# Kernel optimization log

Hardware: AMD Instinct MI355X
Metric: run time of the kernel (lower is better)

Reference implementation:

```python
import jax, jax.numpy as jnp
import numpy as np

D_MODEL = 1024
N_HEADS = 16
D_K = D_MODEL // N_HEADS
B, S = 2, 2048
NEG = -1000000000.0


def setup_inputs() -> dict:
    key = jax.random.key(0)
    ks = jax.random.split(key, 11)
    scale = 1.0 / np.sqrt(D_MODEL)
    inp = {
        'q': jax.random.normal(ks[0], (B, S, D_MODEL), jnp.float32),
        'k': jax.random.normal(ks[1], (B, S, D_MODEL), jnp.float32),
        'v': jax.random.normal(ks[2], (B, S, D_MODEL), jnp.float32),
        'mask': jnp.tril(jnp.ones((S, S), dtype=bool))[None, None],  # causal [1,1,S,S]
        'w_q': jax.random.normal(ks[3], (D_MODEL, D_MODEL), jnp.float32) * scale,
        'b_q': jax.random.normal(ks[4], (D_MODEL,), jnp.float32) * 0.01,
        'w_k': jax.random.normal(ks[5], (D_MODEL, D_MODEL), jnp.float32) * scale,
        'b_k': jax.random.normal(ks[6], (D_MODEL,), jnp.float32) * 0.01,
        'w_v': jax.random.normal(ks[7], (D_MODEL, D_MODEL), jnp.float32) * scale,
        'b_v': jax.random.normal(ks[8], (D_MODEL,), jnp.float32) * 0.01,
        'w_o': jax.random.normal(ks[9], (D_MODEL, D_MODEL), jnp.float32) * scale,
        'b_o': jax.random.normal(ks[10], (D_MODEL,), jnp.float32) * 0.01,
    }
    return inp


def _split_heads(x):
    b, s, _ = x.shape
    return x.reshape(b, s, N_HEADS, D_K).transpose(0, 2, 1, 3)  # [b,h,s,dk]


def reference(q, k, v, mask, w_q, b_q, w_k, b_k, w_v, b_v, w_o, b_o):
    # Linear projections (torch Linear: x @ W.T + b)
    qh = _split_heads(q @ w_q.T + b_q)
    kh = _split_heads(k @ w_k.T + b_k)
    vh = _split_heads(v @ w_v.T + b_v)
    # scaled dot-product attention (dropout is identity in eval)
    scores = jnp.einsum('bhqd,bhkd->bhqk', qh, kh) / jnp.sqrt(jnp.float32(D_K))
    scores = jnp.where(mask, scores, NEG)
    attn_weights = jax.nn.softmax(scores, axis=-1)
    out = jnp.einsum('bhqk,bhkd->bhqd', attn_weights, vh)
    out = out.transpose(0, 2, 1, 3).reshape(q.shape[0], -1, D_MODEL)
    out = out @ w_o.T + b_o
    return out, attn_weights
```

## Files before the change

### kernel.cpp

```cpp
#include <hip/hip_runtime.h>
#include <hip/hip_bf16.h>


#define DM 1024
#define NH 16
#define DKH 64
#define BB 2
#define SS 2048
#define MM (BB*SS)

typedef __bf16 bf16_t;
typedef __bf16 bf16x4 __attribute__((ext_vector_type(4)));
typedef __bf16 bf16x8 __attribute__((ext_vector_type(8)));
typedef float  f32x4  __attribute__((ext_vector_type(4)));

#define EXP2F(x) __builtin_amdgcn_exp2f(x)

__device__ __forceinline__ f32x4 mfma16(bf16x8 a, bf16x8 b, f32x4 c) {
    return __builtin_amdgcn_mfma_f32_16x16x32_bf16(a, b, c, 0, 0, 0);
}
__device__ __forceinline__ bf16x8 cat8(bf16x4 lo, bf16x4 hi) {
    bf16x8 r;
    r[0]=lo[0]; r[1]=lo[1]; r[2]=lo[2]; r[3]=lo[3];
    r[4]=hi[0]; r[5]=hi[1]; r[6]=hi[2]; r[7]=hi[3];
    return r;
}

__device__ __forceinline__ void gload16(const bf16_t* g, bf16_t* l) {
    __builtin_amdgcn_global_load_lds(
        (const __attribute__((address_space(1))) void*)g,
        (__attribute__((address_space(3))) void*)l, 16, 0, 0);
}

__device__ __forceinline__ bf16x8 ldsw(const bf16_t* t, int row, int ch) {
    return *(const bf16x8*)(t + row * 64 + (((ch ^ row) & 7) << 3));
}

__global__ __launch_bounds__(256)
void cvt_bf16(const float* __restrict__ s0, const float* __restrict__ s1,
              const float* __restrict__ s2, const float* __restrict__ s3,
              bf16_t* __restrict__ d0, bf16_t* __restrict__ d1,
              bf16_t* __restrict__ d2, bf16_t* __restrict__ d3)
{
    const float* ss[4] = {s0, s1, s2, s3};
    bf16_t*      dd[4] = {d0, d1, d2, d3};
    const float* s = ss[blockIdx.y];
    bf16_t*      d = dd[blockIdx.y];
    size_t i = (size_t)(blockIdx.x * 256 + threadIdx.x) * 8;
    float4 f0 = *(const float4*)(s + i);
    float4 f1 = *(const float4*)(s + i + 4);
    bf16x8 v;
    v[0]=(bf16_t)f0.x; v[1]=(bf16_t)f0.y; v[2]=(bf16_t)f0.z; v[3]=(bf16_t)f0.w;
    v[4]=(bf16_t)f1.x; v[5]=(bf16_t)f1.y; v[6]=(bf16_t)f1.z; v[7]=(bf16_t)f1.w;
    *(bf16x8*)(d + i) = v;
}

template<int MODE>
__global__ __launch_bounds__(256)
void mha_gemm5(const bf16_t* __restrict__ A, const bf16_t* __restrict__ W,
               const float* __restrict__ bias, void* __restrict__ out)
{
    __shared__ bf16_t As[2][128 * 64];
    __shared__ bf16_t Bs[2][64 * 64];

    const int tid  = threadIdx.x;
    const int lane = tid & 63;
    const int wid  = tid >> 6;
    const int wm = wid >> 1, wn = wid & 1;
    const int bid  = blockIdx.x;
    const int xcd  = bid & 7, slot = bid >> 3;
    const int bm   = xcd * 4 + (slot >> 4);
    const int bn   = slot & 15;
    const int c = lane & 15, g = lane >> 4;
    const int sr = tid >> 3, sch = tid & 7;
    const int scol = ((sch ^ (sr & 7)) << 3);

    f32x4 acc[4][2] = {};

    const bf16_t* Ab = A + (size_t)(bm * 128 + sr) * DM + scol;
    const bf16_t* Wb = W + (size_t)(bn * 64 + sr) * DM + scol;

#define GSTAGE(buf, kt)  do {                                              \
        bf16_t* asl = &As[buf][wid * 512];                                 \
        bf16_t* bsl = &Bs[buf][wid * 512];                                 \
        _Pragma("unroll")                                                  \
        for (int j = 0; j < 4; ++j)                                        \
            gload16(Ab + (size_t)(j * 32) * DM + (kt) * 64, asl + j * 2048);\
        _Pragma("unroll")                                                  \
        for (int j = 0; j < 2; ++j)                                        \
            gload16(Wb + (size_t)(j * 32) * DM + (kt) * 64, bsl + j * 2048);\
    } while (0)

    GSTAGE(0, 0);
    for (int kt = 0; kt < DM / 64; ++kt) {
        const int cur = kt & 1;
        __syncthreads();
        if (kt + 1 < DM / 64) GSTAGE(cur ^ 1, kt + 1);
        const bf16_t* as = As[cur];
        const bf16_t* bs = Bs[cur];
        #pragma unroll
        for (int kh = 0; kh < 2; ++kh) {
            bf16x8 am[4], bw[2];
            #pragma unroll
            for (int f = 0; f < 4; ++f)
                am[f] = ldsw(as, wm * 64 + f * 16 + c, kh * 4 + g);
            #pragma unroll
            for (int f = 0; f < 2; ++f)
                bw[f] = ldsw(bs, wn * 32 + f * 16 + c, kh * 4 + g);
            #pragma unroll
            for (int fm = 0; fm < 4; ++fm)
                #pragma unroll
                for (int fn = 0; fn < 2; ++fn)
                    acc[fm][fn] = mfma16(am[fm], bw[fn], acc[fm][fn]);
        }
    }
#undef GSTAGE

    #pragma unroll
    for (int fm = 0; fm < 4; ++fm) {
        #pragma unroll
        for (int fn = 0; fn < 2; ++fn) {
            const int col = bn * 64 + wn * 32 + fn * 16 + c;
            const float bcol = bias[col];
            if constexpr (MODE == 2) {
                const int h = (col >> 6) & 15, dk = col & 63;
                const int row0 = bm * 128 + wm * 64 + fm * 16 + 4 * g;
                const int b = row0 >> 11, s0 = row0 & (SS - 1);
                bf16x4 pv;
                #pragma unroll
                for (int r = 0; r < 4; ++r) pv[r] = (bf16_t)(acc[fm][fn][r] + bcol);
                size_t idx = ((size_t)((b * NH + h) * DKH + dk)) * SS
                           + ((s0 >> 5) << 5) + g * 8 + (fm & 1) * 4;
                *(bf16x4*)&((bf16_t*)out)[idx] = pv;
            } else {
                #pragma unroll
                for (int r = 0; r < 4; ++r) {
                    const int row = bm * 128 + wm * 64 + fm * 16 + 4 * g + r;
                    float val = acc[fm][fn][r] + bcol;
                    if constexpr (MODE == 3) {
                        __builtin_nontemporal_store(
                            val, &((float*)out)[(size_t)row * DM + col]);
                    } else {
                        if constexpr (MODE == 0)
                            val *= 0.125f * 1.44269504f;
                        const int b = row >> 11, s = row & (SS - 1);
                        const int h = (col >> 6) & 15;
                        const int fnl = (col >> 4) & 3;
                        const int pos = ((fnl >> 1) << 5) + ((c >> 2) << 3)
                                      + ((fnl & 1) << 2) + (c & 3);
                        ((bf16_t*)out)[((size_t)(b * NH + h) * SS + s) * DKH + pos]
                            = (bf16_t)val;
                    }
                }
            }
        }
    }
}

__global__ __launch_bounds__(256)
void mha_attn11(const bf16_t* __restrict__ Qp, const bf16_t* __restrict__ Kp,
                const bf16_t* __restrict__ Vt, float* __restrict__ attn,
                bf16_t* __restrict__ aout)
{
    __shared__ bf16_t Ks[2][8192];
    __shared__ bf16_t Vs[2][8192];

    const int tid = threadIdx.x, lane = tid & 63, w = tid >> 6;
    const int c = lane & 15, g = lane >> 4;
    const int jb = blockIdx.x, bh = blockIdx.y;
    const int b = bh >> 4, h = bh & 15;

    const bf16_t* Qb = Qp + (size_t)bh * SS * DKH;
    const bf16_t* Kb = Kp + (size_t)bh * SS * DKH;
    const bf16_t* Vb = Vt + (size_t)bh * DKH * SS;
    float* attb = attn + (size_t)bh * SS * SS;

    const int sr = tid >> 3, sch = tid & 7;
    const int ssw = ((sch ^ (sr & 7)) << 3);

    #pragma unroll 1
    for (int half = 0; half < 2; ++half) {
        const int qt = half ? (31 - jb) : jb;
        const int q0 = qt * 64, q0w = q0 + w * 16;
        const int ntile = qt + 1;
        const int nr = (ntile + 1) >> 1;

        const bf16_t* qrow = Qb + (size_t)(q0w + c) * DKH;
        const bf16x8 qa0 = *(const bf16x8*)(qrow + g * 8);
        const bf16x8 qa1 = *(const bf16x8*)(qrow + 32 + g * 8);

#define STAGE_K(buf, rr) do {                                               \
        const bf16_t* s0_ = Kb + (size_t)(2 * (rr)) * 4096 + sr * 64 + ssw; \
        gload16(s0_,        &Ks[buf][w * 512]);                             \
        gload16(s0_ + 2048, &Ks[buf][2048 + w * 512]);                      \
        gload16(s0_ + 4096, &Ks[buf][4096 + w * 512]);                      \
        gload16(s0_ + 6144, &Ks[buf][6144 + w * 512]);                      \
    } while (0)

#define STAGE_V(buf, rr) do {                                               \
        const bf16_t* v0_ = Vb + (size_t)sr * SS + (2 * (rr)) * 64 + ssw;   \
        gload16(v0_,                        &Vs[buf][w * 512]);             \
        gload16(v0_ + (size_t)32 * SS,      &Vs[buf][2048 + w * 512]);      \
        gload16(v0_ + 64,                   &Vs[buf][4096 + w * 512]);      \
        gload16(v0_ + (size_t)32 * SS + 64, &Vs[buf][6144 + w * 512]);      \
    } while (0)

        __syncthreads();
        STAGE_K(0, 0);
        float lsum = 0.f;
        for (int rr = 0; rr < nr; ++rr) {
            const int cur = rr & 1;
            __syncthreads();
            if (rr + 1 < nr) STAGE_K(cur ^ 1, rr + 1);
            #pragma unroll
            for (int t = 0; t < 2; ++t) {
                const int kt = 2 * rr + t;
                if (kt < ntile) {
                    const bf16_t* ks = &Ks[cur][t * 4096];
                    f32x4 s[4] = {};
                    #pragma unroll
                    for (int sb = 0; sb < 4; ++sb) {
                        bf16x8 k0 = ldsw(ks, sb * 16 + c, g);
                        bf16x8 k1 = ldsw(ks, sb * 16 + c, 4 | g);
                        s[sb] = mfma16(k0, qa0, s[sb]);
                        s[sb] = mfma16(k1, qa1, s[sb]);
                    }
                    if (kt == qt) {
                        #pragma unroll
                        for (int sb = 0; sb < 4; ++sb)
                            #pragma unroll
                            for (int r = 0; r < 4; ++r)
                                if (sb * 16 + 4 * g + r <= w * 16 + c)
                                    lsum += EXP2F(s[sb][r]);
                    } else {
                        #pragma unroll
                        for (int sb = 0; sb < 4; ++sb)
                            #pragma unroll
                            for (int r = 0; r < 4; ++r)
                                lsum += EXP2F(s[sb][r]);
                    }
                }
            }
        }
        lsum += __shfl_xor(lsum, 16);
        lsum += __shfl_xor(lsum, 32);
        const float invl = 1.f / lsum;

        __syncthreads();
        STAGE_K(0, 0);
        STAGE_V(0, 0);
        f32x4 o[4] = {};
        for (int rr = 0; rr < nr; ++rr) {
            const int cur = rr & 1;
            __syncthreads();
            if (rr + 1 < nr) {
                STAGE_K(cur ^ 1, rr + 1);
                STAGE_V(cur ^ 1, rr + 1);
            }
            #pragma unroll
            for (int t = 0; t < 2; ++t) {
                const int kt = 2 * rr + t;
                if (kt < ntile) {
                    const bf16_t* ks = &Ks[cur][t * 4096];
                    const bf16_t* vs = &Vs[cur][t * 4096];
                    f32x4 s[4] = {};
                    #pragma unroll
                    for (int sb = 0; sb < 4; ++sb) {
                        bf16x8 k0 = ldsw(ks, sb * 16 + c, g);
                        bf16x8 k1 = ldsw(ks, sb * 16 + c, 4 | g);
                        s[sb] = mfma16(k0, qa0, s[sb]);
                        s[sb] = mfma16(k1, qa1, s[sb]);
                    }
                    const bool diag = (kt == qt);
                    bf16x4 pb[4];
                    float* prow = attb + (size_t)(q0w + c) * SS + kt * 64 + 4 * g;
                    #pragma unroll
                    for (int sb = 0; sb < 4; ++sb) {
                        f32x4 pf;
                        #pragma unroll
                        for (int r = 0; r < 4; ++r) {
                            bool msk = diag && (sb * 16 + 4 * g + r > w * 16 + c);
                            float p = msk ? 0.f : EXP2F(s[sb][r]) * invl;
                            pf[r] = p;
                            pb[sb][r] = (bf16_t)p;
                        }
                        *(f32x4*)(prow + sb * 16) = pf;
                    }
                    const bf16x8 pa0 = cat8(pb[0], pb[1]);
                    const bf16x8 pa1 = cat8(pb[2], pb[3]);
                    #pragma unroll
                    for (int fn = 0; fn < 4; ++fn) {
                        bf16x8 v0 = ldsw(vs, fn * 16 + c, g);
                        bf16x8 v1 = ldsw(vs, fn * 16 + c, 4 | g);
                        o[fn] = mfma16(pa0, v0, o[fn]);
                        o[fn] = mfma16(pa1, v1, o[fn]);
                    }
                }
            }
        }
#undef STAGE_K
#undef STAGE_V

        #pragma unroll
        for (int fn = 0; fn < 4; ++fn)
            #pragma unroll
            for (int r = 0; r < 4; ++r)
                aout[(size_t)(b * SS + q0w + 4 * g + r) * DM + h * DKH + fn * 16 + c]
                    = (bf16_t)o[fn][r];

        {
            const int zr = q0 + (tid >> 2);
            f32x4 z = {0.f, 0.f, 0.f, 0.f};
            float* dst = attb + (size_t)zr * SS;
            for (int col = ntile * 64 + (tid & 3) * 4; col < SS; col += 16)
                *(f32x4*)(dst + col) = z;
        }
    }
}

extern "C" void kernel_launch(void* const* d_in, const int* in_sizes, int n_in,
                              void* d_out, int out_size, void* d_ws, size_t ws_size,
                              hipStream_t stream)
{
    const float* q   = (const float*)d_in[0];
    const float* k   = (const float*)d_in[1];
    const float* v   = (const float*)d_in[2];
    const float* w_q = (const float*)d_in[4];
    const float* b_q = (const float*)d_in[5];
    const float* w_k = (const float*)d_in[6];
    const float* b_k = (const float*)d_in[7];
    const float* w_v = (const float*)d_in[8];
    const float* b_v = (const float*)d_in[9];
    const float* w_o = (const float*)d_in[10];
    const float* b_o = (const float*)d_in[11];

    float* out   = (float*)d_out;
    float* attnw = out + (size_t)MM * DM;

    bf16_t* Qp   = (bf16_t*)d_ws;
    bf16_t* Kp   = Qp + (size_t)MM * DM;
    bf16_t* Vt   = Kp + (size_t)MM * DM;
    bf16_t* aout = Vt + (size_t)MM * DM;
    bf16_t* qb   = aout + (size_t)MM * DM;
    bf16_t* kb   = qb + (size_t)MM * DM;
    bf16_t* vb   = kb + (size_t)MM * DM;
    bf16_t* wqb  = vb + (size_t)MM * DM;
    bf16_t* wkb  = wqb + (size_t)DM * DM;
    bf16_t* wvb  = wkb + (size_t)DM * DM;
    bf16_t* wob  = wvb + (size_t)DM * DM;

    cvt_bf16<<<dim3(MM * DM / 2048, 3), 256, 0, stream>>>(q, k, v, q, qb, kb, vb, qb);
    cvt_bf16<<<dim3(DM * DM / 2048, 4), 256, 0, stream>>>(w_q, w_k, w_v, w_o,
                                                          wqb, wkb, wvb, wob);

    mha_gemm5<0><<<512, 256, 0, stream>>>(qb, wqb, b_q, Qp);
    mha_gemm5<1><<<512, 256, 0, stream>>>(kb, wkb, b_k, Kp);
    mha_gemm5<2><<<512, 256, 0, stream>>>(vb, wvb, b_v, Vt);

    mha_attn11<<<dim3(16, BB * NH), 256, 0, stream>>>(Qp, Kp, Vt, attnw, aout);

    mha_gemm5<3><<<512, 256, 0, stream>>>(aout, wob, b_o, out);
}
```

Measured before the change: 256.2 us.

## Process paired query tiles jointly to share K/V staging in attention

The attention kernel used to handle its two query tiles (jb and 31-jb) one after the other, staging K and V from global memory separately for each. It now walks the K/V tiles once for the longer tile and computes both query tiles against each staged tile, so the shorter tile reuses the shared-memory data. This cuts global K/V loads and barrier rounds roughly in half. In exchange it holds two accumulator sets and two Q fragments per thread, which raises register pressure and may lower occupancy.

```diff
diff --git a/kernel.cpp b/kernel.cpp
--- a/kernel.cpp
+++ b/kernel.cpp
@@ -158,7 +158,7 @@
 }
 
 __global__ __launch_bounds__(256)
-void mha_attn11(const bf16_t* __restrict__ Qp, const bf16_t* __restrict__ Kp,
+void mha_attn12(const bf16_t* __restrict__ Qp, const bf16_t* __restrict__ Kp,
                 const bf16_t* __restrict__ Vt, float* __restrict__ attn,
                 bf16_t* __restrict__ aout)
 {
@@ -170,6 +170,12 @@
     const int jb = blockIdx.x, bh = blockIdx.y;
     const int b = bh >> 4, h = bh & 15;
 
+    const int qtA = jb, qtB = 31 - jb;
+    const int q0A = qtA * 64, q0B = qtB * 64;
+    const int q0wA = q0A + w * 16, q0wB = q0B + w * 16;
+    const int ntA = qtA + 1, ntB = qtB + 1;
+    const int nr = (ntB + 1) >> 1;
+
     const bf16_t* Qb = Qp + (size_t)bh * SS * DKH;
     const bf16_t* Kb = Kp + (size_t)bh * SS * DKH;
     const bf16_t* Vb = Vt + (size_t)bh * DKH * SS;
@@ -178,16 +184,12 @@
     const int sr = tid >> 3, sch = tid & 7;
     const int ssw = ((sch ^ (sr & 7)) << 3);
 
-    #pragma unroll 1
-    for (int half = 0; half < 2; ++half) {
-        const int qt = half ? (31 - jb) : jb;
-        const int q0 = qt * 64, q0w = q0 + w * 16;
-        const int ntile = qt + 1;
-        const int nr = (ntile + 1) >> 1;
-
-        const bf16_t* qrow = Qb + (size_t)(q0w + c) * DKH;
-        const bf16x8 qa0 = *(const bf16x8*)(qrow + g * 8);
-        const bf16x8 qa1 = *(const bf16x8*)(qrow + 32 + g * 8);
+    const bf16_t* qrA = Qb + (size_t)(q0wA + c) * DKH;
+    const bf16x8 qaA0 = *(const bf16x8*)(qrA + g * 8);
+    const bf16x8 qaA1 = *(const bf16x8*)(qrA + 32 + g * 8);
+    const bf16_t* qrB = Qb + (size_t)(q0wB + c) * DKH;
+    const bf16x8 qaB0 = *(const bf16x8*)(qrB + g * 8);
+    const bf16x8 qaB1 = *(const bf16x8*)(qrB + 32 + g * 8);
 
 #define STAGE_K(buf, rr) do {                                               \
         const bf16_t* s0_ = Kb + (size_t)(2 * (rr)) * 4096 + sr * 64 + ssw; \
@@ -205,82 +207,111 @@
         gload16(v0_ + (size_t)32 * SS + 64, &Vs[buf][6144 + w * 512]);      \
     } while (0)
 
+    STAGE_K(0, 0);
+    float lsumA = 0.f, lsumB = 0.f;
+    for (int rr = 0; rr < nr; ++rr) {
+        const int cur = rr & 1;
         __syncthreads();
-        STAGE_K(0, 0);
-        float lsum = 0.f;
-        for (int rr = 0; rr < nr; ++rr) {
-            const int cur = rr & 1;
-            __syncthreads();
-            if (rr + 1 < nr) STAGE_K(cur ^ 1, rr + 1);
-            #pragma unroll
-            for (int t = 0; t < 2; ++t) {
-                const int kt = 2 * rr + t;
-                if (kt < ntile) {
-                    const bf16_t* ks = &Ks[cur][t * 4096];
+        if (rr + 1 < nr) STAGE_K(cur ^ 1, rr + 1);
+        #pragma unroll
+        for (int t = 0; t < 2; ++t) {
+            const int kt = 2 * rr + t;
+            if (kt < ntB) {
+                const bf16_t* ks = &Ks[cur][t * 4096];
+                {
                     f32x4 s[4] = {};
                     #pragma unroll
                     for (int sb = 0; sb < 4; ++sb) {
                         bf16x8 k0 = ldsw(ks, sb * 16 + c, g);
                         bf16x8 k1 = ldsw(ks, sb * 16 + c, 4 | g);
-                        s[sb] = mfma16(k0, qa0, s[sb]);
-                        s[sb] = mfma16(k1, qa1, s[sb]);
-                    }
-                    if (kt == qt) {
+                        s[sb] = mfma16(k0, qaB0, s[sb]);
+                        s[sb] = mfma16(k1, qaB1, s[sb]);
+                    }
+                    if (kt == qtB) {
                         #pragma unroll
                         for (int sb = 0; sb < 4; ++sb)
                             #pragma unroll
                             for (int r = 0; r < 4; ++r)
                                 if (sb * 16 + 4 * g + r <= w * 16 + c)
-                                    lsum += EXP2F(s[sb][r]);
+                                    lsumB += EXP2F(s[sb][r]);
                     } else {
                         #pragma unroll
                         for (int sb = 0; sb < 4; ++sb)
                             #pragma unroll
                             for (int r = 0; r < 4; ++r)
-                                lsum += EXP2F(s[sb][r]);
+                                lsumB += EXP2F(s[sb][r]);
+                    }
+                }
+                if (kt < ntA) {
+                    f32x4 s[4] = {};
+                    #pragma unroll
+                    for (int sb = 0; sb < 4; ++sb) {
+                        bf16x8 k0 = ldsw(ks, sb * 16 + c, g);
+                        bf16x8 k1 = ldsw(ks, sb * 16 + c, 4 | g);
+                        s[sb] = mfma16(k0, qaA0, s[sb]);
+                        s[sb] = mfma16(k1, qaA1, s[sb]);
+                    }
+                    if (kt == qtA) {
+                        #pragma unroll
+                        for (int sb = 0; sb < 4; ++sb)
+                            #pragma unroll
+                            for (int r = 0; r < 4; ++r)
+                                if (sb * 16 + 4 * g + r <= w * 16 + c)
+                                    lsumA += EXP2F(s[sb][r]);
+                    } else {
+                        #pragma unroll
+                        for (int sb = 0; sb < 4; ++sb)
+                            #pragma unroll
+                            for (int r = 0; r < 4; ++r)
+                                lsumA += EXP2F(s[sb][r]);
                     }
                 }
             }
         }
-        lsum += __shfl_xor(lsum, 16);
-        lsum += __shfl_xor(lsum, 32);
-        const float invl = 1.f / lsum;
-
+    }
+    lsumA += __shfl_xor(lsumA, 16);
+    lsumA += __shfl_xor(lsumA, 32);
+    lsumB += __shfl_xor(lsumB, 16);
+    lsumB += __shfl_xor(lsumB, 32);
+    const float invlA = 1.f / lsumA;
+    const float invlB = 1.f / lsumB;
+
+    __syncthreads();
+    STAGE_K(0, 0);
+    STAGE_V(0, 0);
+    f32x4 oA[4] = {}, oB[4] = {};
+    for (int rr = 0; rr < nr; ++rr) {
+        const int cur = rr & 1;
         __syncthreads();
-        STAGE_K(0, 0);
-        STAGE_V(0, 0);
-        f32x4 o[4] = {};
-        for (int rr = 0; rr < nr; ++rr) {
-            const int cur = rr & 1;
-            __syncthreads();
-            if (rr + 1 < nr) {
-                STAGE_K(cur ^ 1, rr + 1);
-                STAGE_V(cur ^ 1, rr + 1);
-            }
-            #pragma unroll
-            for (int t = 0; t < 2; ++t) {
-                const int kt = 2 * rr + t;
-                if (kt < ntile) {
-                    const bf16_t* ks = &Ks[cur][t * 4096];
-                    const bf16_t* vs = &Vs[cur][t * 4096];
+        if (rr + 1 < nr) {
+            STAGE_K(cur ^ 1, rr + 1);
+            STAGE_V(cur ^ 1, rr + 1);
+        }
+        #pragma unroll
+        for (int t = 0; t < 2; ++t) {
+            const int kt = 2 * rr + t;
+            if (kt < ntB) {
+                const bf16_t* ks = &Ks[cur][t * 4096];
+                const bf16_t* vs = &Vs[cur][t * 4096];
+                {
                     f32x4 s[4] = {};
                     #pragma unroll
                     for (int sb = 0; sb < 4; ++sb) {
                         bf16x8 k0 = ldsw(ks, sb * 16 + c, g);
                         bf16x8 k1 = ldsw(ks, sb * 16 + c, 4 | g);
-                        s[sb] = mfma16(k0, qa0, s[sb]);
-                        s[sb] = mfma16(k1, qa1, s[sb]);
-                    }
-                    const bool diag = (kt == qt);
+                        s[sb] = mfma16(k0, qaB0, s[sb]);
+                        s[sb] = mfma16(k1, qaB1, s[sb]);
+                    }
+                    const bool diag = (kt == qtB);
                     bf16x4 pb[4];
-                    float* prow = attb + (size_t)(q0w + c) * SS + kt * 64 + 4 * g;
+                    float* prow = attb + (size_t)(q0wB + c) * SS + kt * 64 + 4 * g;
                     #pragma unroll
                     for (int sb = 0; sb < 4; ++sb) {
                         f32x4 pf;
                         #pragma unroll
                         for (int r = 0; r < 4; ++r) {
                             bool msk = diag && (sb * 16 + 4 * g + r > w * 16 + c);
-                            float p = msk ? 0.f : EXP2F(s[sb][r]) * invl;
+                            float p = msk ? 0.f : EXP2F(s[sb][r]) * invlB;
                             pf[r] = p;
                             pb[sb][r] = (bf16_t)p;
                         }
@@ -292,27 +323,72 @@
                     for (int fn = 0; fn < 4; ++fn) {
                         bf16x8 v0 = ldsw(vs, fn * 16 + c, g);
                         bf16x8 v1 = ldsw(vs, fn * 16 + c, 4 | g);
-                        o[fn] = mfma16(pa0, v0, o[fn]);
-                        o[fn] = mfma16(pa1, v1, o[fn]);
+                        oB[fn] = mfma16(pa0, v0, oB[fn]);
+                        oB[fn] = mfma16(pa1, v1, oB[fn]);
+                    }
+                }
+                if (kt < ntA) {
+                    f32x4 s[4] = {};
+                    #pragma unroll
+                    for (int sb = 0; sb < 4; ++sb) {
+                        bf16x8 k0 = ldsw(ks, sb * 16 + c, g);
+                        bf16x8 k1 = ldsw(ks, sb * 16 + c, 4 | g);
+                        s[sb] = mfma16(k0, qaA0, s[sb]);
+                        s[sb] = mfma16(k1, qaA1, s[sb]);
+                    }
+                    const bool diag = (kt == qtA);
+                    bf16x4 pb[4];
+                    float* prow = attb + (size_t)(q0wA + c) * SS + kt * 64 + 4 * g;
+                    #pragma unroll
+                    for (int sb = 0; sb < 4; ++sb) {
+                        f32x4 pf;
+                        #pragma unroll
+                        for (int r = 0; r < 4; ++r) {
+                            bool msk = diag && (sb * 16 + 4 * g + r > w * 16 + c);
+                            float p = msk ? 0.f : EXP2F(s[sb][r]) * invlA;
+                            pf[r] = p;
+                            pb[sb][r] = (bf16_t)p;
+                        }
+                        *(f32x4*)(prow + sb * 16) = pf;
+                    }
+                    const bf16x8 pa0 = cat8(pb[0], pb[1]);
+                    const bf16x8 pa1 = cat8(pb[2], pb[3]);
+                    #pragma unroll
+                    for (int fn = 0; fn < 4; ++fn) {
+                        bf16x8 v0 = ldsw(vs, fn * 16 + c, g);
+                        bf16x8 v1 = ldsw(vs, fn * 16 + c, 4 | g);
+                        oA[fn] = mfma16(pa0, v0, oA[fn]);
+                        oA[fn] = mfma16(pa1, v1, oA[fn]);
                     }
                 }
             }
         }
+    }
 #undef STAGE_K
 #undef STAGE_V
 
+    #pragma unroll
+    for (int fn = 0; fn < 4; ++fn)
         #pragma unroll
-        for (int fn = 0; fn < 4; ++fn)
-            #pragma unroll
-            for (int r = 0; r < 4; ++r)
-                aout[(size_t)(b * SS + q0w + 4 * g + r) * DM + h * DKH + fn * 16 + c]
-                    = (bf16_t)o[fn][r];
-
+        for (int r = 0; r < 4; ++r) {
+            aout[(size_t)(b * SS + q0wB + 4 * g + r) * DM + h * DKH + fn * 16 + c]
+                = (bf16_t)oB[fn][r];
+            aout[(size_t)(b * SS + q0wA + 4 * g + r) * DM + h * DKH + fn * 16 + c]
+                = (bf16_t)oA[fn][r];
+        }
+
+    {
+        f32x4 z = {0.f, 0.f, 0.f, 0.f};
         {
-            const int zr = q0 + (tid >> 2);
-            f32x4 z = {0.f, 0.f, 0.f, 0.f};
+            const int zr = q0A + (tid >> 2);
             float* dst = attb + (size_t)zr * SS;
-            for (int col = ntile * 64 + (tid & 3) * 4; col < SS; col += 16)
+            for (int col = ntA * 64 + (tid & 3) * 4; col < SS; col += 16)
+                *(f32x4*)(dst + col) = z;
+        }
+        {
+            const int zr = q0B + (tid >> 2);
+            float* dst = attb + (size_t)zr * SS;
+            for (int col = ntB * 64 + (tid & 3) * 4; col < SS; col += 16)
                 *(f32x4*)(dst + col) = z;
         }
     }
@@ -357,7 +433,7 @@
     mha_gemm5<1><<<512, 256, 0, stream>>>(kb, wkb, b_k, Kp);
     mha_gemm5<2><<<512, 256, 0, stream>>>(vb, wvb, b_v, Vt);
 
-    mha_attn11<<<dim3(16, BB * NH), 256, 0, stream>>>(Qp, Kp, Vt, attnw, aout);
+    mha_attn12<<<dim3(16, BB * NH), 256, 0, stream>>>(Qp, Kp, Vt, attnw, aout);
 
     mha_gemm5<3><<<512, 256, 0, stream>>>(aout, wob, b_o, out);
 }
```

Measured after the change: 247.0 us. 1.04x faster.
